# Optimization experiments

Measured on AMD Instinct MI355X. Metric: run time of the kernel, lower is better.

## Reference

```python
import jax, jax.numpy as jnp
import numpy as np

D_MODEL = 256
POOL = 3
SR = 2  # sampling_ratio
TEMP = 10000.0


def pos_grid(D, H, W):
    """2D sine-cos positional encoding, (D,H,W). pos_y channels first, pos_x second."""
    dq = D // 4
    dim_t = TEMP ** (2.0 * (jnp.arange(dq) // 2).astype(jnp.float32) / dq)

    def enc(coord):  # (L,) -> (L, 2*dq), interleaved sin/cos
        p = coord[:, None] / dim_t
        return jnp.stack([jnp.sin(p), jnp.cos(p)], axis=-1).reshape(coord.shape[0], -1)

    py = enc(jnp.linspace(0.0, 1.0, H))  # (H, 2dq)
    px = enc(jnp.linspace(0.0, 1.0, W))  # (W, 2dq)
    pos = jnp.concatenate([
        jnp.broadcast_to(py[:, None, :], (H, W, 2 * dq)),
        jnp.broadcast_to(px[None, :, :], (H, W, 2 * dq)),
    ], axis=-1)  # (H, W, D)
    return jnp.transpose(pos, (2, 0, 1))  # (D, H, W)


def proj_pos(x, Wp, bp):
    """1x1 conv projection to D then add 2D pos enc. x: (B,C,H,W) -> (B,D,H,W)."""
    y = jnp.einsum('bchw,dc->bdhw', x, Wp) + bp[None, :, None, None]
    return y + pos_grid(Wp.shape[0], x.shape[2], x.shape[3])[None]


def roi_align_mean(feat, bidx, boxes, scale):
    """torchvision roi_align (aligned=True, sampling_ratio=SR, output=POOLxPOOL)
    followed by mean over the pooled grid. feat (B,D,H,W), boxes (N,4) xyxy -> (N,D).
    Since every bin averages SR*SR samples, mean over bins == mean over all samples."""
    B, D, H, W = feat.shape
    f = jnp.transpose(feat, (0, 2, 3, 1))  # (B,H,W,D)
    x1 = boxes[:, 0] * scale - 0.5
    y1 = boxes[:, 1] * scale - 0.5
    x2 = boxes[:, 2] * scale - 0.5
    y2 = boxes[:, 3] * scale - 0.5
    bw = (x2 - x1) / POOL
    bh = (y2 - y1) / POOL
    # sample offsets within roi, in units of bin size: (POOL*SR,)
    off = (jnp.arange(POOL, dtype=jnp.float32)[:, None]
           + (jnp.arange(SR, dtype=jnp.float32)[None, :] + 0.5) / SR).reshape(-1)
    ys = y1[:, None] + bh[:, None] * off  # (N,S) with S = POOL*SR
    xs = x1[:, None] + bw[:, None] * off

    def coords(c, size):
        valid = (c >= -1.0) & (c <= size)
        c = jnp.clip(c, 0.0, None)
        cl = jnp.minimum(jnp.floor(c).astype(jnp.int32), size - 1)
        ch = jnp.minimum(cl + 1, size - 1)
        return cl, ch, c - cl, valid

    yl, yh, ly, vy = coords(ys, H)
    xl, xh, lx, vx = coords(xs, W)
    hy, hx = 1.0 - ly, 1.0 - lx

    def gather(yy, xx):  # -> (N,S,S,D)
        return f[bidx[:, None, None], yy[:, :, None], xx[:, None, :]]

    v = (hy[:, :, None, None] * hx[:, None, :, None] * gather(yl, xl)
         + hy[:, :, None, None] * lx[:, None, :, None] * gather(yl, xh)
         + ly[:, :, None, None] * hx[:, None, :, None] * gather(yh, xl)
         + ly[:, :, None, None] * lx[:, None, :, None] * gather(yh, xh))
    mask = (vy[:, :, None] & vx[:, None, :])[..., None]
    v = jnp.where(mask, v, 0.0)
    return v.mean(axis=(1, 2))  # (N, D)


def token_mlp(tok, ln_g, ln_b, W1, b1, W2, b2):
    m = tok.mean(-1, keepdims=True)
    var = jnp.mean((tok - m) ** 2, -1, keepdims=True)
    h = (tok - m) / jnp.sqrt(var + 1e-5) * ln_g + ln_b
    h = jax.nn.gelu(h @ W1.T + b1, approximate=False)  # torch nn.GELU default = exact
    return h @ W2.T + b2


def setup_inputs():
    key = jax.random.key(0)
    ks = jax.random.split(key, 16)
    B, K, D = 8, 100, D_MODEL
    p3 = jax.random.normal(ks[0], (B, 512, 128, 128), jnp.float32)
    p4 = jax.random.normal(ks[1], (B, 1024, 64, 64), jnp.float32)
    p5 = jax.random.normal(ks[2], (B, 2048, 32, 32), jnp.float32)
    # valid xyxy boxes inside a 1024x1024 frame
    x1 = jax.random.uniform(ks[3], (B, K, 1)) * 880.0
    y1 = jax.random.uniform(ks[4], (B, K, 1)) * 880.0
    bw = jax.random.uniform(ks[5], (B, K, 1)) * 128.0 + 8.0
    bh = jax.random.uniform(ks[6], (B, K, 1)) * 128.0 + 8.0
    boxes = jnp.concatenate([x1, y1, x1 + bw, y1 + bh], axis=-1)

    def lin(k, o, i):
        return (jax.random.normal(k, (o, i), jnp.float32) / np.sqrt(i)).astype(jnp.float32)

    return dict(
        p3=p3, p4=p4, p5=p5, boxes=boxes,
        W3=lin(ks[7], D, 512), b3=jnp.zeros((D,), jnp.float32),
        W4=lin(ks[8], D, 1024), b4=jnp.zeros((D,), jnp.float32),
        W5=lin(ks[9], D, 2048), b5=jnp.zeros((D,), jnp.float32),
        ln_g=jnp.ones((D,), jnp.float32), ln_b=jnp.zeros((D,), jnp.float32),
        W1=lin(ks[10], D, D), b1=jnp.zeros((D,), jnp.float32),
        W2=lin(ks[11], D, D), b2=jnp.zeros((D,), jnp.float32),
        input_w=1024, input_h=1024,
    )


def reference(p3, p4, p5, boxes, W3, b3, W4, b4, W5, b5, ln_g, ln_b, W1, b1, W2, b2, input_w, input_h):
    B, K = boxes.shape[0], boxes.shape[1]
    bidx = jnp.repeat(jnp.arange(B, dtype=jnp.int32), K)  # (B*K,)
    flat = boxes.reshape(-1, 4)
    tok = jnp.zeros((B * K, D_MODEL), jnp.float32)
    for feat, Wp, bp in ((p3, W3, b3), (p4, W4, b4), (p5, W5, b5)):
        y = proj_pos(feat, Wp, bp)
        s = min(y.shape[3] / (input_w + 1e-6), y.shape[2] / (input_h + 1e-6))
        tok = tok + roi_align_mean(y, bidx, flat, s)
    tok = token_mlp(tok, ln_g, ln_b, W1, b1, W2, b2)
    return tok.reshape(B, K, D_MODEL)
```

## Files before the change

### kernel.cpp

```cpp
#include <hip/hip_runtime.h>
#include <hip/hip_fp16.h>
#include <math.h>

#ifndef INT_MAX
#define INT_MAX 0x7fffffff
#endif

typedef __attribute__((ext_vector_type(8))) _Float16 f16x8;
typedef __attribute__((ext_vector_type(4))) float   f32x4;


__device__ __forceinline__ float gelu_exact(float x) {
    return 0.5f * x * (1.0f + erff(x * 0.70710678118654752f));
}

__global__ __launch_bounds__(256)
void build_wt3_kernel(const float* __restrict__ W3, const float* __restrict__ W4,
                      const float* __restrict__ W5, const float* __restrict__ W1,
                      const float* __restrict__ W2,
                      __half* __restrict__ WF3, __half* __restrict__ WF4,
                      __half* __restrict__ WF5,
                      float* __restrict__ W1T, float* __restrict__ W2T)
{
    const int bidx = blockIdx.x;
    const int tid  = threadIdx.x;
    if (bidx < 448) {
        const int c = bidx * 256 + tid;
        const float* Wsrc; __half* dst; int K, c0;
        if (c < 16384)      { Wsrc = W3; dst = WF3; K = 512;  c0 = c; }
        else if (c < 49152) { Wsrc = W4; dst = WF4; K = 1024; c0 = c - 16384; }
        else                { Wsrc = W5; dst = WF5; K = 2048; c0 = c - 49152; }
        const int t  = c0 >> 10;
        const int r  = c0 & 1023;
        const int d  = r >> 2;
        const int lg = r & 3;
        const float* src = Wsrc + (size_t)d * K + t * 32 + lg * 8;
        f16x8 hv;
        #pragma unroll
        for (int j = 0; j < 8; ++j) hv[j] = (_Float16)src[j];
        *(f16x8*)(dst + (size_t)c0 * 8) = hv;
    } else if (bidx < 704) {
        const int k = bidx - 448;
        W1T[(size_t)k * 256 + tid] = W1[(size_t)tid * 256 + k];
    } else {
        const int k = bidx - 704;
        W2T[(size_t)k * 256 + tid] = W2[(size_t)tid * 256 + k];
    }
}

__global__ __launch_bounds__(256)
void roi_setup2_kernel(const float* __restrict__ boxes,
                       const float* __restrict__ b3, const float* __restrict__ b4,
                       const float* __restrict__ b5,
                       const int* __restrict__ iw_p, const int* __restrict__ ih_p,
                       float* __restrict__ SREC, float* __restrict__ P)
{
    const int n   = blockIdx.x;
    const int s   = blockIdx.y;
    const int tid = threadIdx.x;

    int H, W;
    const float* bp;
    if (s == 0)      { H = 128; W = 128; bp = b3; }
    else if (s == 1) { H = 64;  W = 64;  bp = b4; }
    else             { H = 32;  W = 32;  bp = b5; }

    __shared__ float wy[32];
    __shared__ float wx[48];
    __shared__ int   sh_r0, sh_rs, sh_x0, sh_xs;
    __shared__ float sh_syc, sh_sxc;

    if (tid < 32)              wy[tid]      = 0.0f;
    if (tid >= 32 && tid < 80) wx[tid - 32] = 0.0f;
    __syncthreads();

    const float scale = fminf((float)W / ((float)(*iw_p) + 1e-6f),
                              (float)H / ((float)(*ih_p) + 1e-6f));
    float* rec = &SREC[(size_t)(n * 3 + s) * 64];

    if (tid == 0) {
        float c1 = boxes[(size_t)n * 4 + 1] * scale - 0.5f;
        float c2 = boxes[(size_t)n * 4 + 3] * scale - 0.5f;
        float bs = (c2 - c1) / 3.0f;
        int   yls[6], yhs[6], vv[6];
        float lys[6];
        int r0 = INT_MAX; float cnt = 0.0f;
        #pragma unroll
        for (int i = 0; i < 6; ++i) {
            float off = 0.25f + 0.5f * (float)i;
            float ys  = c1 + bs * off;
            int v = (ys >= -1.0f) && (ys <= (float)H);
            float yc = fmaxf(ys, 0.0f);
            int yl = (int)floorf(yc); if (yl > H - 1) yl = H - 1;
            int yh = yl + 1;          if (yh > H - 1) yh = H - 1;
            float ly = yc - (float)yl;
            yls[i] = yl; yhs[i] = yh; lys[i] = ly; vv[i] = v;
            if (v) { r0 = min(r0, yl); cnt += 1.0f; }
        }
        if (r0 == INT_MAX) r0 = 0;
        int rmax = 0;
        #pragma unroll
        for (int i = 0; i < 6; ++i) if (vv[i]) {
            int a = min(yls[i] - r0, 31);
            int h = min(yhs[i] - r0, 31);
            wy[a] += 1.0f - lys[i];
            wy[h] += lys[i];
            rmax = max(rmax, h);
        }
        sh_r0 = r0; sh_rs = rmax + 1; sh_syc = cnt;
        int cntn = 0;
        for (int r = 0; r <= rmax && cntn < 12; ++r) {
            if (wy[r] != 0.0f) {
                rec[4 + cntn]  = (float)(r0 + r);
                rec[16 + cntn] = wy[r];
                ++cntn;
            }
        }
        rec[0] = (float)cntn;
    }
    if (tid == 1) {
        float c1 = boxes[(size_t)n * 4 + 0] * scale - 0.5f;
        float c2 = boxes[(size_t)n * 4 + 2] * scale - 0.5f;
        float bs = (c2 - c1) / 3.0f;
        int   xls[6], xhs[6], vv[6];
        float lxs[6];
        int x0r = INT_MAX; float cnt = 0.0f;
        #pragma unroll
        for (int i = 0; i < 6; ++i) {
            float off = 0.25f + 0.5f * (float)i;
            float xs  = c1 + bs * off;
            int v = (xs >= -1.0f) && (xs <= (float)W);
            float xc = fmaxf(xs, 0.0f);
            int xl = (int)floorf(xc); if (xl > W - 1) xl = W - 1;
            int xh = xl + 1;          if (xh > W - 1) xh = W - 1;
            float lx = xc - (float)xl;
            xls[i] = xl; xhs[i] = xh; lxs[i] = lx; vv[i] = v;
            if (v) { x0r = min(x0r, xl); cnt += 1.0f; }
        }
        if (x0r == INT_MAX) x0r = 0;
        int imax = 0;
        #pragma unroll
        for (int i = 0; i < 6; ++i) if (vv[i]) {
            int a = min(xls[i] - x0r, 47);
            int h = min(xhs[i] - x0r, 47);
            wx[a] += 1.0f - lxs[i];
            wx[h] += lxs[i];
            imax = max(imax, h);
        }
        sh_x0 = x0r; sh_xs = imax + 1; sh_sxc = cnt;
        int cntn = 0;
        for (int j = 0; j <= imax && cntn < 12; ++j) {
            if (wx[j] != 0.0f) {
                rec[28 + cntn] = (float)(x0r + j);
                rec[40 + cntn] = wx[j];
                ++cntn;
            }
        }
        rec[1] = (float)cntn;
    }
    __syncthreads();

    const int r0 = sh_r0, rs = sh_rs, x0 = sh_x0, xsr = sh_xs;

    {
        const int d = tid;
        const float syc = sh_syc, sxc = sh_sxc;
        float val;
        if (d < 128) {
            int   t     = d >> 2;
            float invf  = expf(-(float)t * (logf(10000.0f) / 32.0f));
            float istep = 1.0f / (float)(H - 1);
            float sum = 0.0f;
            for (int r = 0; r < rs; ++r) {
                float w = wy[r];
                if (w != 0.0f) {
                    float ang = (float)(r0 + r) * istep * invf;
                    float sn, cs; sincosf(ang, &sn, &cs);
                    sum = fmaf(w, (d & 1) ? cs : sn, sum);
                }
            }
            val = sxc * sum;
        } else {
            int   d2    = d - 128;
            int   t     = d2 >> 2;
            float invf  = expf(-(float)t * (logf(10000.0f) / 32.0f));
            float istep = 1.0f / (float)(W - 1);
            float sum = 0.0f;
            for (int j = 0; j < xsr; ++j) {
                float w = wx[j];
                if (w != 0.0f) {
                    float ang = (float)(x0 + j) * istep * invf;
                    float sn, cs; sincosf(ang, &sn, &cs);
                    sum = fmaf(w, (d & 1) ? cs : sn, sum);
                }
            }
            val = syc * sum;
        }
        float cnt = syc * sxc;
        P[((size_t)n * 3 + s) * 256 + d] = (val + cnt * bp[d]) * (1.0f / 36.0f);
    }
}

__global__ __launch_bounds__(512, 2)
void proj5_kernel(const float* __restrict__ p3, const float* __restrict__ p4,
                  const float* __restrict__ p5,
                  const __half* __restrict__ WF3, const __half* __restrict__ WF4,
                  const __half* __restrict__ WF5,
                  __half* __restrict__ F3, __half* __restrict__ F4,
                  __half* __restrict__ F5,
                  int n5, int n4)
{
    const int bid = blockIdx.x;
    const float* feat; const __half* WF; __half* F;
    int C, HW, m0;
    if (bid < n5)           { C = 2048; HW = 1024;  feat = p5; WF = WF5; F = F5; m0 = bid * 64; }
    else if (bid < n5 + n4) { C = 1024; HW = 4096;  feat = p4; WF = WF4; F = F4; m0 = (bid - n5) * 64; }
    else                    { C = 512;  HW = 16384; feat = p3; WF = WF3; F = F3; m0 = (bid - n5 - n4) * 64; }

    const int tid = threadIdx.x;
    const int wv  = tid >> 6;
    const int l   = tid & 63;
    const int lm  = l & 15;
    const int lg  = l >> 4;
    const int dq  = wv & 3;
    const int ph  = wv >> 2;
    const int b    = m0 / HW;
    const int pos0 = m0 % HW;
    const int nk   = C >> 5;

    const float* a0 = feat + (size_t)b * C * HW + pos0 + ph * 32 + lm;
    const float* a1 = a0 + 16;
    const __half* wbase = WF + ((size_t)(dq * 64 + lm) * 4 + lg) * 8;

    f32x4 acc[8];
    #pragma unroll
    for (int i = 0; i < 8; ++i) acc[i] = (f32x4){0.f, 0.f, 0.f, 0.f};

    float a0c[8], a1c[8], a0n[8], a1n[8];
    f16x8 bc[4], bn[4];

    #pragma unroll
    for (int j = 0; j < 8; ++j) {
        const size_t ko = (size_t)(lg * 8 + j) * HW;
        a0c[j] = a0[ko]; a1c[j] = a1[ko];
    }
    #pragma unroll
    for (int j = 0; j < 8; ++j) {
        const size_t ko = (size_t)(32 + lg * 8 + j) * HW;
        a0n[j] = a0[ko]; a1n[j] = a1[ko];
    }
    #pragma unroll
    for (int nt = 0; nt < 4; ++nt) bc[nt] = *(const f16x8*)(wbase + nt * 512);
    #pragma unroll
    for (int nt = 0; nt < 4; ++nt) bn[nt] = *(const f16x8*)(wbase + 8192 + nt * 512);

    for (int t = 0; t < nk; t += 2) {
        {
            f16x8 af0, af1;
            #pragma unroll
            for (int j = 0; j < 8; ++j) {
                af0[j] = (_Float16)a0c[j];
                af1[j] = (_Float16)a1c[j];
            }
            if (t + 2 < nk) {
                const int k0 = (t + 2) * 32;
                #pragma unroll
                for (int j = 0; j < 8; ++j) {
                    const size_t ko = (size_t)(k0 + lg * 8 + j) * HW;
                    a0c[j] = a0[ko]; a1c[j] = a1[ko];
                }
            }
            #pragma unroll
            for (int nt = 0; nt < 4; ++nt) {
                acc[nt]     = __builtin_amdgcn_mfma_f32_16x16x32_f16(af0, bc[nt], acc[nt],     0, 0, 0);
                acc[nt + 4] = __builtin_amdgcn_mfma_f32_16x16x32_f16(af1, bc[nt], acc[nt + 4], 0, 0, 0);
            }
            if (t + 2 < nk) {
                const __half* wb = wbase + (size_t)(t + 2) * 8192;
                #pragma unroll
                for (int nt = 0; nt < 4; ++nt) bc[nt] = *(const f16x8*)(wb + nt * 512);
            }
        }
        {
            f16x8 af0, af1;
            #pragma unroll
            for (int j = 0; j < 8; ++j) {
                af0[j] = (_Float16)a0n[j];
                af1[j] = (_Float16)a1n[j];
            }
            if (t + 3 < nk) {
                const int k0 = (t + 3) * 32;
                #pragma unroll
                for (int j = 0; j < 8; ++j) {
                    const size_t ko = (size_t)(k0 + lg * 8 + j) * HW;
                    a0n[j] = a0[ko]; a1n[j] = a1[ko];
                }
            }
            #pragma unroll
            for (int nt = 0; nt < 4; ++nt) {
                acc[nt]     = __builtin_amdgcn_mfma_f32_16x16x32_f16(af0, bn[nt], acc[nt],     0, 0, 0);
                acc[nt + 4] = __builtin_amdgcn_mfma_f32_16x16x32_f16(af1, bn[nt], acc[nt + 4], 0, 0, 0);
            }
            if (t + 3 < nk) {
                const __half* wb = wbase + (size_t)(t + 3) * 8192;
                #pragma unroll
                for (int nt = 0; nt < 4; ++nt) bn[nt] = *(const f16x8*)(wb + nt * 512);
            }
        }
    }

    #pragma unroll
    for (int mt = 0; mt < 2; ++mt) {
        #pragma unroll
        for (int nt = 0; nt < 4; ++nt) {
            #pragma unroll
            for (int i = 0; i < 4; ++i) {
                const int px = pos0 + ph * 32 + mt * 16 + lg * 4 + i;
                const int d  = dq * 64 + nt * 16 + lm;
                F[((size_t)b * HW + px) * 256 + d] = __float2half(acc[nt + mt * 4][i]);
            }
        }
    }
}

__global__ __launch_bounds__(256)
void sample2_kernel(const __half* __restrict__ F3, const __half* __restrict__ F4,
                    const __half* __restrict__ F5,
                    const float* __restrict__ SREC, const float* __restrict__ P,
                    float* __restrict__ tokp, int K100)
{
    const int n = blockIdx.x;
    const int s = blockIdx.y;
    const int d = threadIdx.x;
    const int b = n / K100;

    __shared__ float rsh[64];
    if (d < 64) rsh[d] = SREC[(size_t)(n * 3 + s) * 64 + d];
    __syncthreads();

    const __half* F; int HW, W;
    if (s == 0)      { F = F3; HW = 16384; W = 128; }
    else if (s == 1) { F = F4; HW = 4096;  W = 64; }
    else             { F = F5; HW = 1024;  W = 32; }

    const int ny = (int)rsh[0];
    const int nx = (int)rsh[1];
    const size_t base = (size_t)b * HW * 256 + d;

    float acc = 0.0f;
    for (int i = 0; i < ny; ++i) {
        const int   row = (int)rsh[4 + i];
        const float wyv = rsh[16 + i];
        const size_t rb = base + (size_t)(row * W) * 256;
        float rsum = 0.0f;
        for (int j = 0; j < nx; ++j) {
            const int   col = (int)rsh[28 + j];
            const float wxv = rsh[40 + j];
            rsum = fmaf(wxv, __half2float(F[rb + (size_t)col * 256]), rsum);
        }
        acc = fmaf(wyv, rsum, acc);
    }
    tokp[(size_t)(n * 3 + s) * 256 + d] = acc * (1.0f / 36.0f)
                                        + P[(size_t)(n * 3 + s) * 256 + d];
}

__global__ __launch_bounds__(256)
void mlp2_kernel(const float* __restrict__ tokp,
                 const float* __restrict__ lng, const float* __restrict__ lnb,
                 const float* __restrict__ W1T, const float* __restrict__ b1,
                 const float* __restrict__ W2T, const float* __restrict__ b2,
                 float* __restrict__ out, int N)
{
    const int n0  = blockIdx.x * 8;
    const int tid = threadIdx.x;

    __shared__ float tokl[8][257];
    __shared__ float hl[8][257];
    __shared__ float mval[8], rstd[8];

    #pragma unroll
    for (int t = 0; t < 8; ++t) {
        const size_t nb = (size_t)(n0 + t) * 3 * 256 + tid;
        tokl[t][tid] = tokp[nb] + tokp[nb + 256] + tokp[nb + 512];
    }
    __syncthreads();

    const int wv = tid >> 6, lane = tid & 63;
    for (int t = wv; t < 8; t += 4) {
        float x0 = tokl[t][lane], x1 = tokl[t][lane + 64];
        float x2 = tokl[t][lane + 128], x3 = tokl[t][lane + 192];
        float sm = x0 + x1 + x2 + x3;
        float sq = x0 * x0 + x1 * x1 + x2 * x2 + x3 * x3;
        #pragma unroll
        for (int o = 32; o; o >>= 1) { sm += __shfl_xor(sm, o); sq += __shfl_xor(sq, o); }
        if (lane == 0) {
            float m   = sm * (1.0f / 256.0f);
            float var = sq * (1.0f / 256.0f) - m * m;
            mval[t] = m;
            rstd[t] = rsqrtf(var + 1e-5f);
        }
    }
    __syncthreads();

    const float g = lng[tid], be = lnb[tid];
    #pragma unroll
    for (int t = 0; t < 8; ++t)
        hl[t][tid] = (tokl[t][tid] - mval[t]) * rstd[t] * g + be;
    __syncthreads();

    float acc[8];
    const float bb1 = b1[tid];
    #pragma unroll
    for (int t = 0; t < 8; ++t) acc[t] = bb1;
    for (int k = 0; k < 256; ++k) {
        float w = W1T[(size_t)k * 256 + tid];
        #pragma unroll
        for (int t = 0; t < 8; ++t) acc[t] = fmaf(hl[t][k], w, acc[t]);
    }
    __syncthreads();
    #pragma unroll
    for (int t = 0; t < 8; ++t) tokl[t][tid] = gelu_exact(acc[t]);
    __syncthreads();

    const float bb2 = b2[tid];
    #pragma unroll
    for (int t = 0; t < 8; ++t) acc[t] = bb2;
    for (int k = 0; k < 256; ++k) {
        float w = W2T[(size_t)k * 256 + tid];
        #pragma unroll
        for (int t = 0; t < 8; ++t) acc[t] = fmaf(tokl[t][k], w, acc[t]);
    }
    #pragma unroll
    for (int t = 0; t < 8; ++t)
        out[(size_t)(n0 + t) * 256 + tid] = acc[t];
}


__global__ __launch_bounds__(256)
void build_wt_kernel(const float* __restrict__ W3, const float* __restrict__ W4,
                     const float* __restrict__ W5, const float* __restrict__ W1,
                     const float* __restrict__ W2,
                     float* __restrict__ WT, float* __restrict__ W1T,
                     float* __restrict__ W2T)
{
    int k = blockIdx.x;
    int d = threadIdx.x;
    if (k < 512)       WT[(size_t)k * 256 + d]          = W3[(size_t)d * 512  + k];
    else if (k < 1536) WT[(size_t)k * 256 + d]          = W4[(size_t)d * 1024 + (k - 512)];
    else if (k < 3584) WT[(size_t)k * 256 + d]          = W5[(size_t)d * 2048 + (k - 1536)];
    else if (k < 3840) W1T[(size_t)(k - 3584) * 256 + d] = W1[(size_t)d * 256 + (k - 3584)];
    else               W2T[(size_t)(k - 3840) * 256 + d] = W2[(size_t)d * 256 + (k - 3840)];
}

__global__ __launch_bounds__(256)
void roi_setup_kernel(const float* __restrict__ boxes,
                      const float* __restrict__ b3, const float* __restrict__ b4,
                      const float* __restrict__ b5,
                      const int* __restrict__ iw_p, const int* __restrict__ ih_p,
                      float* __restrict__ WREC, float* __restrict__ P)
{
    const int n   = blockIdx.x;
    const int s   = blockIdx.y;
    const int tid = threadIdx.x;

    int H, W;
    const float* bp;
    if (s == 0)      { H = 128; W = 128; bp = b3; }
    else if (s == 1) { H = 64;  W = 64;  bp = b4; }
    else             { H = 32;  W = 32;  bp = b5; }

    __shared__ float wy[32];
    __shared__ float wx[48];
    __shared__ int   sh_r0, sh_rs, sh_x0, sh_nc;
    __shared__ float sh_syc, sh_sxc;

    if (tid < 32)                 wy[tid]      = 0.0f;
    if (tid >= 32 && tid < 80)    wx[tid - 32] = 0.0f;
    __syncthreads();

    const float scale = fminf((float)W / ((float)(*iw_p) + 1e-6f),
                              (float)H / ((float)(*ih_p) + 1e-6f));

    if (tid == 0) {
        float c1 = boxes[(size_t)n * 4 + 1] * scale - 0.5f;
        float c2 = boxes[(size_t)n * 4 + 3] * scale - 0.5f;
        float bs = (c2 - c1) / 3.0f;
        int   yls[6], yhs[6], vv[6];
        float lys[6];
        int r0 = INT_MAX; float cnt = 0.0f;
        #pragma unroll
        for (int i = 0; i < 6; ++i) {
            float off = 0.25f + 0.5f * (float)i;
            float ys  = c1 + bs * off;
            int v = (ys >= -1.0f) && (ys <= (float)H);
            float yc = fmaxf(ys, 0.0f);
            int yl = (int)floorf(yc); if (yl > H - 1) yl = H - 1;
            int yh = yl + 1;          if (yh > H - 1) yh = H - 1;
            float ly = yc - (float)yl;
            yls[i] = yl; yhs[i] = yh; lys[i] = ly; vv[i] = v;
            if (v) { r0 = min(r0, yl); cnt += 1.0f; }
        }
        if (r0 == INT_MAX) r0 = 0;
        int rmax = 0;
        #pragma unroll
        for (int i = 0; i < 6; ++i) if (vv[i]) {
            int a = min(yls[i] - r0, 31);
            int h = min(yhs[i] - r0, 31);
            wy[a] += 1.0f - lys[i];
            wy[h] += lys[i];
            rmax = max(rmax, h);
        }
        sh_r0 = r0; sh_rs = rmax + 1; sh_syc = cnt;
    }
    if (tid == 1) {
        float c1 = boxes[(size_t)n * 4 + 0] * scale - 0.5f;
        float c2 = boxes[(size_t)n * 4 + 2] * scale - 0.5f;
        float bs = (c2 - c1) / 3.0f;
        int   xls[6], xhs[6], vv[6];
        float lxs[6];
        int x0r = INT_MAX; float cnt = 0.0f;
        #pragma unroll
        for (int i = 0; i < 6; ++i) {
            float off = 0.25f + 0.5f * (float)i;
            float xs  = c1 + bs * off;
            int v = (xs >= -1.0f) && (xs <= (float)W);
            float xc = fmaxf(xs, 0.0f);
            int xl = (int)floorf(xc); if (xl > W - 1) xl = W - 1;
            int xh = xl + 1;          if (xh > W - 1) xh = W - 1;
            float lx = xc - (float)xl;
            xls[i] = xl; xhs[i] = xh; lxs[i] = lx; vv[i] = v;
            if (v) { x0r = min(x0r, xl); cnt += 1.0f; }
        }
        if (x0r == INT_MAX) x0r = 0;
        int x0 = x0r & ~15;
        int imax = 0;
        #pragma unroll
        for (int i = 0; i < 6; ++i) if (vv[i]) {
            int a = min(xls[i] - x0, 47);
            int h = min(xhs[i] - x0, 47);
            wx[a] += 1.0f - lxs[i];
            wx[h] += lxs[i];
            imax = max(imax, h);
        }
        int nc = imax / 16 + 1;
        int ncmax = (W - x0) >> 4;
        nc = min(nc, ncmax);
        sh_x0 = x0; sh_nc = max(nc, 1); sh_sxc = cnt;
    }
    __syncthreads();

    const int r0 = sh_r0, rs = sh_rs, x0 = sh_x0, nc = sh_nc;

    float* rec = &WREC[(size_t)(n * 3 + s) * 96];
    if (tid < 32)                 rec[tid]      = wy[tid];
    else if (tid < 80)            rec[tid]      = wx[tid - 32];
    else if (tid == 80)           rec[80]       = (float)r0;
    else if (tid == 81)           rec[81]       = (float)rs;
    else if (tid == 82)           rec[82]       = (float)x0;
    else if (tid == 83)           rec[83]       = (float)nc;
    else if (tid == 84)           rec[84]       = sh_syc;
    else if (tid == 85)           rec[85]       = sh_sxc;

    {
        const int d = tid;
        const float syc = sh_syc, sxc = sh_sxc;
        float val;
        if (d < 128) {
            int   t     = d >> 2;
            float invf  = expf(-(float)t * (logf(10000.0f) / 32.0f));
            float istep = 1.0f / (float)(H - 1);
            float sum = 0.0f;
            for (int r = 0; r < rs; ++r) {
                float w = wy[r];
                float ang = (float)(r0 + r) * istep * invf;
                float sn, cs; sincosf(ang, &sn, &cs);
                sum = fmaf(w, (d & 1) ? cs : sn, sum);
            }
            val = sxc * sum;
        } else {
            int   d2    = d - 128;
            int   t     = d2 >> 2;
            float invf  = expf(-(float)t * (logf(10000.0f) / 32.0f));
            float istep = 1.0f / (float)(W - 1);
            float sum = 0.0f;
            int nx = nc << 4;
            for (int j = 0; j < nx; ++j) {
                float w = wx[j];
                if (w != 0.0f) {
                    float ang = (float)(x0 + j) * istep * invf;
                    float sn, cs; sincosf(ang, &sn, &cs);
                    sum = fmaf(w, (d & 1) ? cs : sn, sum);
                }
            }
            val = syc * sum;
        }
        float cnt = syc * sxc;
        P[((size_t)n * 3 + s) * 256 + d] = (val + cnt * bp[d]) * (1.0f / 36.0f);
    }
}

__global__ __launch_bounds__(256)
void roi_gather_kernel(const float* __restrict__ p3, const float* __restrict__ p4,
                       const float* __restrict__ p5,
                       const float* __restrict__ WREC,
                       float* __restrict__ G, int K)
{
    const int yc  = blockIdx.x;
    const int n   = blockIdx.y;
    const int tid = threadIdx.x;

    int s, chunk;
    if (yc < 8)       { s = 0; chunk = yc; }
    else if (yc < 24) { s = 1; chunk = yc - 8; }
    else              { s = 2; chunk = yc - 24; }

    int C, H, W, koff;
    const float* feat;
    if (s == 0)      { C = 512;  H = 128; W = 128; koff = 0;    feat = p3; }
    else if (s == 1) { C = 1024; H = 64;  W = 64;  koff = 512;  feat = p4; }
    else             { C = 2048; H = 32;  W = 32;  koff = 1536; feat = p5; }
    const int HW = H * W;
    const int b  = n / K;

    __shared__ float sh[96];
    if (tid < 96) sh[tid] = WREC[(size_t)(n * 3 + s) * 96 + tid];
    __syncthreads();

    const int r0 = (int)sh[80];
    const int rs = (int)sh[81];
    const int x0 = (int)sh[82];
    const int nc = (int)sh[83];

    const int c    = chunk * 64 + (tid >> 2);
    const int slot = tid & 3;

    const float* fp = feat + (size_t)b * C * HW + (size_t)c * HW
                    + (size_t)r0 * W + x0 + slot * 4;

    float acc = 0.0f;
    for (int ch = 0; ch < nc; ++ch) {
        const float4 wxv = *(const float4*)&sh[32 + (ch << 4) + slot * 4];
        const float* a = fp + (ch << 4);
        float4 ra = make_float4(0.f, 0.f, 0.f, 0.f);
        int r = 0;
        for (; r + 4 <= rs; r += 4) {
            const float4 v0 = *(const float4*)(a + (size_t)(r + 0) * W);
            const float4 v1 = *(const float4*)(a + (size_t)(r + 1) * W);
            const float4 v2 = *(const float4*)(a + (size_t)(r + 2) * W);
            const float4 v3 = *(const float4*)(a + (size_t)(r + 3) * W);
            const float w0 = sh[r], w1 = sh[r + 1], w2 = sh[r + 2], w3 = sh[r + 3];
            ra.x = fmaf(w0, v0.x, ra.x); ra.y = fmaf(w0, v0.y, ra.y);
            ra.z = fmaf(w0, v0.z, ra.z); ra.w = fmaf(w0, v0.w, ra.w);
            ra.x = fmaf(w1, v1.x, ra.x); ra.y = fmaf(w1, v1.y, ra.y);
            ra.z = fmaf(w1, v1.z, ra.z); ra.w = fmaf(w1, v1.w, ra.w);
            ra.x = fmaf(w2, v2.x, ra.x); ra.y = fmaf(w2, v2.y, ra.y);
            ra.z = fmaf(w2, v2.z, ra.z); ra.w = fmaf(w2, v2.w, ra.w);
            ra.x = fmaf(w3, v3.x, ra.x); ra.y = fmaf(w3, v3.y, ra.y);
            ra.z = fmaf(w3, v3.z, ra.z); ra.w = fmaf(w3, v3.w, ra.w);
        }
        for (; r < rs; ++r) {
            const float4 v = *(const float4*)(a + (size_t)r * W);
            const float w = sh[r];
            ra.x = fmaf(w, v.x, ra.x); ra.y = fmaf(w, v.y, ra.y);
            ra.z = fmaf(w, v.z, ra.z); ra.w = fmaf(w, v.w, ra.w);
        }
        float dsum = ra.x * wxv.x + ra.y * wxv.y + ra.z * wxv.z + ra.w * wxv.w;
        acc += dsum;
    }
    acc += __shfl_xor(acc, 1, 4);
    acc += __shfl_xor(acc, 2, 4);
    if (slot == 0)
        G[(size_t)n * 3584 + koff + c] = acc * (1.0f / 36.0f);
}

__global__ __launch_bounds__(256)
void proj_gemm_kernel(const float* __restrict__ G, const float* __restrict__ WT,
                      float* __restrict__ part, int N)
{
    const int n0  = blockIdx.x * 8;
    const int kc  = blockIdx.y;
    const int tid = threadIdx.x;

    __shared__ float gl[8][128];
    float acc[8];
    #pragma unroll
    for (int t = 0; t < 8; ++t) acc[t] = 0.0f;

    const int kbase = kc * 512;
    const int lt  = tid >> 5;
    const int lc  = (tid & 31) * 4;

    for (int sub = 0; sub < 4; ++sub) {
        const float4 g4 = *(const float4*)&G[(size_t)(n0 + lt) * 3584 + kbase + sub * 128 + lc];
        *(float4*)&gl[lt][lc] = g4;
        __syncthreads();
        const float* wtp = &WT[(size_t)(kbase + sub * 128) * 256 + tid];
        #pragma unroll 4
        for (int k = 0; k < 128; ++k) {
            float w = wtp[(size_t)k * 256];
            #pragma unroll
            for (int t = 0; t < 8; ++t) acc[t] = fmaf(gl[t][k], w, acc[t]);
        }
        __syncthreads();
    }
    #pragma unroll
    for (int t = 0; t < 8; ++t)
        part[((size_t)kc * N + n0 + t) * 256 + tid] = acc[t];
}

__global__ __launch_bounds__(256)
void mlp_kernel(const float* __restrict__ part, const float* __restrict__ P,
                const float* __restrict__ lng, const float* __restrict__ lnb,
                const float* __restrict__ W1T, const float* __restrict__ b1,
                const float* __restrict__ W2T, const float* __restrict__ b2,
                float* __restrict__ out, int N)
{
    const int n0  = blockIdx.x * 8;
    const int tid = threadIdx.x;

    __shared__ float tokl[8][257];
    __shared__ float hl[8][257];
    __shared__ float mval[8], rstd[8];

    #pragma unroll
    for (int t = 0; t < 8; ++t) {
        const int n = n0 + t;
        float v = 0.0f;
        #pragma unroll
        for (int c = 0; c < 7; ++c) v += part[((size_t)c * N + n) * 256 + tid];
        #pragma unroll
        for (int s = 0; s < 3; ++s) v += P[((size_t)n * 3 + s) * 256 + tid];
        tokl[t][tid] = v;
    }
    __syncthreads();

    const int wv = tid >> 6, lane = tid & 63;
    for (int t = wv; t < 8; t += 4) {
        float x0 = tokl[t][lane], x1 = tokl[t][lane + 64];
        float x2 = tokl[t][lane + 128], x3 = tokl[t][lane + 192];
        float sm = x0 + x1 + x2 + x3;
        float sq = x0 * x0 + x1 * x1 + x2 * x2 + x3 * x3;
        #pragma unroll
        for (int o = 32; o; o >>= 1) { sm += __shfl_xor(sm, o); sq += __shfl_xor(sq, o); }
        if (lane == 0) {
            float m   = sm * (1.0f / 256.0f);
            float var = sq * (1.0f / 256.0f) - m * m;
            mval[t] = m;
            rstd[t] = rsqrtf(var + 1e-5f);
        }
    }
    __syncthreads();

    const float g = lng[tid], be = lnb[tid];
    #pragma unroll
    for (int t = 0; t < 8; ++t)
        hl[t][tid] = (tokl[t][tid] - mval[t]) * rstd[t] * g + be;
    __syncthreads();

    float acc[8];
    const float bb1 = b1[tid];
    #pragma unroll
    for (int t = 0; t < 8; ++t) acc[t] = bb1;
    for (int k = 0; k < 256; ++k) {
        float w = W1T[(size_t)k * 256 + tid];
        #pragma unroll
        for (int t = 0; t < 8; ++t) acc[t] = fmaf(hl[t][k], w, acc[t]);
    }
    __syncthreads();
    #pragma unroll
    for (int t = 0; t < 8; ++t) tokl[t][tid] = gelu_exact(acc[t]);
    __syncthreads();

    const float bb2 = b2[tid];
    #pragma unroll
    for (int t = 0; t < 8; ++t) acc[t] = bb2;
    for (int k = 0; k < 256; ++k) {
        float w = W2T[(size_t)k * 256 + tid];
        #pragma unroll
        for (int t = 0; t < 8; ++t) acc[t] = fmaf(tokl[t][k], w, acc[t]);
    }
    #pragma unroll
    for (int t = 0; t < 8; ++t)
        out[(size_t)(n0 + t) * 256 + tid] = acc[t];
}

extern "C" void kernel_launch(void* const* d_in, const int* in_sizes, int n_in,
                              void* d_out, int out_size, void* d_ws, size_t ws_size,
                              hipStream_t stream)
{
    const float* p3    = (const float*)d_in[0];
    const float* p4    = (const float*)d_in[1];
    const float* p5    = (const float*)d_in[2];
    const float* boxes = (const float*)d_in[3];
    const float* W3    = (const float*)d_in[4];
    const float* b3    = (const float*)d_in[5];
    const float* W4    = (const float*)d_in[6];
    const float* b4    = (const float*)d_in[7];
    const float* W5    = (const float*)d_in[8];
    const float* b5    = (const float*)d_in[9];
    const float* lng   = (const float*)d_in[10];
    const float* lnb   = (const float*)d_in[11];
    const float* W1    = (const float*)d_in[12];
    const float* b1    = (const float*)d_in[13];
    const float* W2    = (const float*)d_in[14];
    const float* b2    = (const float*)d_in[15];
    const int*   iw    = (const int*)d_in[16];
    const int*   ih    = (const int*)d_in[17];

    const int B = in_sizes[0] / (512 * 128 * 128);
    const int N = out_size / 256;
    const int K100 = N / B;

    float* out = (float*)d_out;

    const size_t szF3   = (size_t)B * 16384 * 256 * 2;
    const size_t szF4   = (size_t)B * 4096  * 256 * 2;
    const size_t szF5   = (size_t)B * 1024  * 256 * 2;
    const size_t szWF   = (size_t)3584 * 256 * 2;
    const size_t szSREC = (size_t)N * 3 * 64 * 4;
    const size_t szP    = (size_t)N * 3 * 256 * 4;
    const size_t szTok  = (size_t)N * 3 * 256 * 4;
    const size_t szWT12 = (size_t)256 * 256 * 4;
    const size_t need_new = szF3 + szF4 + szF5 + szWF + szSREC + szP + szTok + 2 * szWT12;

    if (ws_size >= need_new) {
        char* w = (char*)d_ws;
        __half* F3   = (__half*)w;            w += szF3;
        __half* F4   = (__half*)w;            w += szF4;
        __half* F5   = (__half*)w;            w += szF5;
        __half* WF   = (__half*)w;            w += szWF;
        float*  SREC = (float*)w;             w += szSREC;
        float*  P    = (float*)w;             w += szP;
        float*  tokp = (float*)w;             w += szTok;
        float*  W1T  = (float*)w;             w += szWT12;
        float*  W2T  = (float*)w;             w += szWT12;

        __half* WF3 = WF;
        __half* WF4 = WF + 131072;
        __half* WF5 = WF + 393216;

        const int n5 = B * 1024  / 64;
        const int n4 = B * 4096  / 64;
        const int n3 = B * 16384 / 64;

        build_wt3_kernel<<<960, 256, 0, stream>>>(W3, W4, W5, W1, W2,
                                                  WF3, WF4, WF5, W1T, W2T);
        roi_setup2_kernel<<<dim3(N, 3), 256, 0, stream>>>(boxes, b3, b4, b5, iw, ih, SREC, P);
        proj5_kernel<<<n5 + n4 + n3, 512, 0, stream>>>(p3, p4, p5, WF3, WF4, WF5,
                                                       F3, F4, F5, n5, n4);
        sample2_kernel<<<dim3(N, 3), 256, 0, stream>>>(F3, F4, F5, SREC, P, tokp, K100);
        mlp2_kernel<<<N / 8, 256, 0, stream>>>(tokp, lng, lnb, W1T, b1, W2T, b2, out, N);
    } else {
        float* G    = (float*)d_ws;
        float* P    = G + (size_t)N * 3584;
        float* WT   = P + (size_t)N * 3 * 256;
        float* W1T  = WT + (size_t)3584 * 256;
        float* W2T  = W1T + (size_t)256 * 256;
        float* part = W2T + (size_t)256 * 256;
        float* WREC = part + (size_t)7 * N * 256;

        build_wt_kernel<<<4096, 256, 0, stream>>>(W3, W4, W5, W1, W2, WT, W1T, W2T);
        roi_setup_kernel<<<dim3(N, 3), 256, 0, stream>>>(boxes, b3, b4, b5, iw, ih, WREC, P);
        roi_gather_kernel<<<dim3(56, N), 256, 0, stream>>>(p3, p4, p5, WREC, G, K100);
        proj_gemm_kernel<<<dim3(N / 8, 7), 256, 0, stream>>>(G, WT, part, N);
        mlp_kernel<<<N / 8, 256, 0, stream>>>(part, P, lng, lnb, W1T, b1, W2T, b2, out, N);
    }
}
```

Baseline: 326.3 us.

## Stage projection activations through LDS via global_load_lds double buffering

The projection GEMM kernel stops loading fp32 activations with strided per-lane global loads into registers. It now uses async global_load_lds copies into a double-buffered shared tile, then reads float4s back out of LDS in MFMA fragment order. The intent is better coalesced global access and fewer registers, which removes the register prefetch arrays. In exchange it adds block-wide barriers on every k-step and drops the min-blocks launch bound, so occupancy and synchronization behavior change.

```diff
diff --git a/kernel.cpp b/kernel.cpp
--- a/kernel.cpp
+++ b/kernel.cpp
@@ -9,6 +9,11 @@
 typedef __attribute__((ext_vector_type(8))) _Float16 f16x8;
 typedef __attribute__((ext_vector_type(4))) float   f32x4;
 
+
+#define GLD4(src, dst)                                                        \
+    __builtin_amdgcn_global_load_lds(                                         \
+        (const __attribute__((address_space(1))) unsigned int*)(const void*)(src), \
+        (__attribute__((address_space(3))) unsigned int*)(void*)(dst), 4, 0, 0)
 
 __device__ __forceinline__ float gelu_exact(float x) {
     return 0.5f * x * (1.0f + erff(x * 0.70710678118654752f));
@@ -201,8 +206,8 @@
     }
 }
 
-__global__ __launch_bounds__(512, 2)
-void proj5_kernel(const float* __restrict__ p3, const float* __restrict__ p4,
+__global__ __launch_bounds__(512)
+void proj6_kernel(const float* __restrict__ p3, const float* __restrict__ p4,
                   const float* __restrict__ p5,
                   const __half* __restrict__ WF3, const __half* __restrict__ WF4,
                   const __half* __restrict__ WF5,
@@ -228,48 +233,63 @@
     const int pos0 = m0 % HW;
     const int nk   = C >> 5;
 
-    const float* a0 = feat + (size_t)b * C * HW + pos0 + ph * 32 + lm;
-    const float* a1 = a0 + 16;
+    __shared__ float sa[2][2048];
+
+    const float* a_st = feat + (size_t)b * C * HW + pos0
+                      + (size_t)(l & 7) * HW + (wv << 3) + (l >> 3);
+    const size_t kstep_str = (size_t)32 * HW;
+    const size_t ktile_str = (size_t)8 * HW;
+
     const __half* wbase = WF + ((size_t)(dq * 64 + lm) * 4 + lg) * 8;
 
+    const int pxq0 = ph * 32 + lm;
+    const int pxq1 = pxq0 + 16;
+    const int ro0 = (((pxq0 >> 3) << 2) + lg) * 64 + ((pxq0 & 7) << 3);
+    const int ro1 = (((pxq1 >> 3) << 2) + lg) * 64 + ((pxq1 & 7) << 3);
+
     f32x4 acc[8];
     #pragma unroll
     for (int i = 0; i < 8; ++i) acc[i] = (f32x4){0.f, 0.f, 0.f, 0.f};
 
-    float a0c[8], a1c[8], a0n[8], a1n[8];
     f16x8 bc[4], bn[4];
 
-    #pragma unroll
-    for (int j = 0; j < 8; ++j) {
-        const size_t ko = (size_t)(lg * 8 + j) * HW;
-        a0c[j] = a0[ko]; a1c[j] = a1[ko];
-    }
-    #pragma unroll
-    for (int j = 0; j < 8; ++j) {
-        const size_t ko = (size_t)(32 + lg * 8 + j) * HW;
-        a0n[j] = a0[ko]; a1n[j] = a1[ko];
+    {
+        const float* s = a_st;
+        float* d0 = &sa[0][(wv * 4) * 64];
+        GLD4(s,                 d0);
+        GLD4(s + ktile_str,     d0 + 64);
+        GLD4(s + 2 * ktile_str, d0 + 128);
+        GLD4(s + 3 * ktile_str, d0 + 192);
     }
     #pragma unroll
     for (int nt = 0; nt < 4; ++nt) bc[nt] = *(const f16x8*)(wbase + nt * 512);
     #pragma unroll
     for (int nt = 0; nt < 4; ++nt) bn[nt] = *(const f16x8*)(wbase + 8192 + nt * 512);
+    __syncthreads();
 
     for (int t = 0; t < nk; t += 2) {
         {
+            const float* s = a_st + (size_t)(t + 1) * kstep_str;
+            float* d0 = &sa[1][(wv * 4) * 64];
+            GLD4(s,                 d0);
+            GLD4(s + ktile_str,     d0 + 64);
+            GLD4(s + 2 * ktile_str, d0 + 128);
+            GLD4(s + 3 * ktile_str, d0 + 192);
+
+            const float* bufc = sa[0];
+            const float4 va = *(const float4*)(bufc + ro0);
+            const float4 vb = *(const float4*)(bufc + ro0 + 4);
+            const float4 vc = *(const float4*)(bufc + ro1);
+            const float4 vd = *(const float4*)(bufc + ro1 + 4);
             f16x8 af0, af1;
-            #pragma unroll
-            for (int j = 0; j < 8; ++j) {
-                af0[j] = (_Float16)a0c[j];
-                af1[j] = (_Float16)a1c[j];
-            }
-            if (t + 2 < nk) {
-                const int k0 = (t + 2) * 32;
-                #pragma unroll
-                for (int j = 0; j < 8; ++j) {
-                    const size_t ko = (size_t)(k0 + lg * 8 + j) * HW;
-                    a0c[j] = a0[ko]; a1c[j] = a1[ko];
-                }
-            }
+            af0[0] = (_Float16)va.x; af0[1] = (_Float16)va.y;
+            af0[2] = (_Float16)va.z; af0[3] = (_Float16)va.w;
+            af0[4] = (_Float16)vb.x; af0[5] = (_Float16)vb.y;
+            af0[6] = (_Float16)vb.z; af0[7] = (_Float16)vb.w;
+            af1[0] = (_Float16)vc.x; af1[1] = (_Float16)vc.y;
+            af1[2] = (_Float16)vc.z; af1[3] = (_Float16)vc.w;
+            af1[4] = (_Float16)vd.x; af1[5] = (_Float16)vd.y;
+            af1[6] = (_Float16)vd.z; af1[7] = (_Float16)vd.w;
             #pragma unroll
             for (int nt = 0; nt < 4; ++nt) {
                 acc[nt]     = __builtin_amdgcn_mfma_f32_16x16x32_f16(af0, bc[nt], acc[nt],     0, 0, 0);
@@ -280,22 +300,31 @@
                 #pragma unroll
                 for (int nt = 0; nt < 4; ++nt) bc[nt] = *(const f16x8*)(wb + nt * 512);
             }
+            __syncthreads();
         }
         {
+            if (t + 2 < nk) {
+                const float* s = a_st + (size_t)(t + 2) * kstep_str;
+                float* d0 = &sa[0][(wv * 4) * 64];
+                GLD4(s,                 d0);
+                GLD4(s + ktile_str,     d0 + 64);
+                GLD4(s + 2 * ktile_str, d0 + 128);
+                GLD4(s + 3 * ktile_str, d0 + 192);
+            }
+            const float* bufc = sa[1];
+            const float4 va = *(const float4*)(bufc + ro0);
+            const float4 vb = *(const float4*)(bufc + ro0 + 4);
+            const float4 vc = *(const float4*)(bufc + ro1);
+            const float4 vd = *(const float4*)(bufc + ro1 + 4);
             f16x8 af0, af1;
-            #pragma unroll
-            for (int j = 0; j < 8; ++j) {
-                af0[j] = (_Float16)a0n[j];
-                af1[j] = (_Float16)a1n[j];
-            }
-            if (t + 3 < nk) {
-                const int k0 = (t + 3) * 32;
-                #pragma unroll
-                for (int j = 0; j < 8; ++j) {
-                    const size_t ko = (size_t)(k0 + lg * 8 + j) * HW;
-                    a0n[j] = a0[ko]; a1n[j] = a1[ko];
-                }
-            }
+            af0[0] = (_Float16)va.x; af0[1] = (_Float16)va.y;
+            af0[2] = (_Float16)va.z; af0[3] = (_Float16)va.w;
+            af0[4] = (_Float16)vb.x; af0[5] = (_Float16)vb.y;
+            af0[6] = (_Float16)vb.z; af0[7] = (_Float16)vb.w;
+            af1[0] = (_Float16)vc.x; af1[1] = (_Float16)vc.y;
+            af1[2] = (_Float16)vc.z; af1[3] = (_Float16)vc.w;
+            af1[4] = (_Float16)vd.x; af1[5] = (_Float16)vd.y;
+            af1[6] = (_Float16)vd.z; af1[7] = (_Float16)vd.w;
             #pragma unroll
             for (int nt = 0; nt < 4; ++nt) {
                 acc[nt]     = __builtin_amdgcn_mfma_f32_16x16x32_f16(af0, bn[nt], acc[nt],     0, 0, 0);
@@ -306,6 +335,7 @@
                 #pragma unroll
                 for (int nt = 0; nt < 4; ++nt) bn[nt] = *(const f16x8*)(wb + nt * 512);
             }
+            __syncthreads();
         }
     }
 
@@ -846,7 +876,7 @@
         build_wt3_kernel<<<960, 256, 0, stream>>>(W3, W4, W5, W1, W2,
                                                   WF3, WF4, WF5, W1T, W2T);
         roi_setup2_kernel<<<dim3(N, 3), 256, 0, stream>>>(boxes, b3, b4, b5, iw, ih, SREC, P);
-        proj5_kernel<<<n5 + n4 + n3, 512, 0, stream>>>(p3, p4, p5, WF3, WF4, WF5,
+        proj6_kernel<<<n5 + n4 + n3, 512, 0, stream>>>(p3, p4, p5, WF3, WF4, WF5,
                                                        F3, F4, F5, n5, n4);
         sample2_kernel<<<dim3(N, 3), 256, 0, stream>>>(F3, F4, F5, SREC, P, tokp, K100);
         mlp2_kernel<<<N / 8, 256, 0, stream>>>(tokp, lng, lnb, W1T, b1, W2T, b2, out, N);
```

After: 341.2 us, median of 2. 1.05x slower.

## Stage projection activations through double-buffered swizzled LDS with float4 global loads

Applied to the files above, without the earlier changes.

In the projection GEMM kernel, each thread used to issue many scalar strided global loads for its MFMA A-fragments. It now loads one float4 of the 32-channel x 64-pixel activation tile per thread, writes it into a double-buffered, XOR-swizzled shared-memory tile, and reads the A-fragments from LDS. The goal is coalesced, vectorised global reads and fewer load instructions. In exchange it adds a barrier per K-step, some LDS traffic and shared-memory use, which could lower occupancy.

```diff
diff --git a/kernel.cpp b/kernel.cpp
--- a/kernel.cpp
+++ b/kernel.cpp
@@ -202,7 +202,7 @@
 }
 
 __global__ __launch_bounds__(512, 2)
-void proj5_kernel(const float* __restrict__ p3, const float* __restrict__ p4,
+void proj8_kernel(const float* __restrict__ p3, const float* __restrict__ p4,
                   const float* __restrict__ p5,
                   const __half* __restrict__ WF3, const __half* __restrict__ WF4,
                   const __half* __restrict__ WF5,
@@ -226,86 +226,86 @@
     const int ph  = wv >> 2;
     const int b    = m0 / HW;
     const int pos0 = m0 % HW;
-    const int nk   = C >> 5;
-
-    const float* a0 = feat + (size_t)b * C * HW + pos0 + ph * 32 + lm;
-    const float* a1 = a0 + 16;
+    const int nsub = C >> 5;
+
+    __shared__ float sa[2][32 * 68];
+
+    const int kk  = tid >> 4;
+    const int pxg = tid & 15;
+    const float* ag = feat + (size_t)b * C * HW + pos0 + pxg * 4 + (size_t)kk * HW;
+    const size_t sstr = (size_t)32 * HW;
+    const int wcol = 4 * (pxg ^ (kk >> 3));
+    const int woff = kk * 68 + wcol;
+
     const __half* wbase = WF + ((size_t)(dq * 64 + lm) * 4 + lg) * 8;
 
+    const int pxq0 = ph * 32 + lm;
+    const int pxq1 = pxq0 + 16;
+    const int rbase0 = lg * 8 * 68 + (pxq0 ^ (4 * lg));
+    const int rbase1 = lg * 8 * 68 + (pxq1 ^ (4 * lg));
+
     f32x4 acc[8];
     #pragma unroll
     for (int i = 0; i < 8; ++i) acc[i] = (f32x4){0.f, 0.f, 0.f, 0.f};
 
-    float a0c[8], a1c[8], a0n[8], a1n[8];
     f16x8 bc[4], bn[4];
-
-    #pragma unroll
-    for (int j = 0; j < 8; ++j) {
-        const size_t ko = (size_t)(lg * 8 + j) * HW;
-        a0c[j] = a0[ko]; a1c[j] = a1[ko];
-    }
-    #pragma unroll
-    for (int j = 0; j < 8; ++j) {
-        const size_t ko = (size_t)(32 + lg * 8 + j) * HW;
-        a0n[j] = a0[ko]; a1n[j] = a1[ko];
-    }
+    float4 vh;
+
+    {
+        const float4 v0 = *(const float4*)ag;
+        *(float4*)&sa[0][woff] = v0;
+    }
+    vh = *(const float4*)(ag + sstr);
     #pragma unroll
     for (int nt = 0; nt < 4; ++nt) bc[nt] = *(const f16x8*)(wbase + nt * 512);
     #pragma unroll
     for (int nt = 0; nt < 4; ++nt) bn[nt] = *(const f16x8*)(wbase + 8192 + nt * 512);
-
-    for (int t = 0; t < nk; t += 2) {
+    __syncthreads();
+
+    for (int s = 0; s < nsub; s += 2) {
         {
+            *(float4*)&sa[1][woff] = vh;
+            if (s + 2 < nsub) vh = *(const float4*)(ag + (size_t)(s + 2) * sstr);
+
+            const float* buf = sa[0];
             f16x8 af0, af1;
             #pragma unroll
-            for (int j = 0; j < 8; ++j) {
-                af0[j] = (_Float16)a0c[j];
-                af1[j] = (_Float16)a1c[j];
-            }
-            if (t + 2 < nk) {
-                const int k0 = (t + 2) * 32;
-                #pragma unroll
-                for (int j = 0; j < 8; ++j) {
-                    const size_t ko = (size_t)(k0 + lg * 8 + j) * HW;
-                    a0c[j] = a0[ko]; a1c[j] = a1[ko];
-                }
-            }
+            for (int j = 0; j < 8; ++j) af0[j] = (_Float16)buf[rbase0 + j * 68];
+            #pragma unroll
+            for (int j = 0; j < 8; ++j) af1[j] = (_Float16)buf[rbase1 + j * 68];
             #pragma unroll
             for (int nt = 0; nt < 4; ++nt) {
                 acc[nt]     = __builtin_amdgcn_mfma_f32_16x16x32_f16(af0, bc[nt], acc[nt],     0, 0, 0);
                 acc[nt + 4] = __builtin_amdgcn_mfma_f32_16x16x32_f16(af1, bc[nt], acc[nt + 4], 0, 0, 0);
             }
-            if (t + 2 < nk) {
-                const __half* wb = wbase + (size_t)(t + 2) * 8192;
+            if (s + 2 < nsub) {
+                const __half* wb = wbase + (size_t)(s + 2) * 8192;
                 #pragma unroll
                 for (int nt = 0; nt < 4; ++nt) bc[nt] = *(const f16x8*)(wb + nt * 512);
             }
+            __syncthreads();
         }
         {
+            if (s + 2 < nsub) *(float4*)&sa[0][woff] = vh;
+            if (s + 3 < nsub) vh = *(const float4*)(ag + (size_t)(s + 3) * sstr);
+
+            const float* buf = sa[1];
             f16x8 af0, af1;
             #pragma unroll
-            for (int j = 0; j < 8; ++j) {
-                af0[j] = (_Float16)a0n[j];
-                af1[j] = (_Float16)a1n[j];
-            }
-            if (t + 3 < nk) {
-                const int k0 = (t + 3) * 32;
-                #pragma unroll
-                for (int j = 0; j < 8; ++j) {
-                    const size_t ko = (size_t)(k0 + lg * 8 + j) * HW;
-                    a0n[j] = a0[ko]; a1n[j] = a1[ko];
-                }
-            }
+            for (int j = 0; j < 8; ++j) af0[j] = (_Float16)buf[rbase0 + j * 68];
+            #pragma unroll
+            for (int j = 0; j < 8; ++j) af1[j] = (_Float16)buf[rbase1 + j * 68];
             #pragma unroll
             for (int nt = 0; nt < 4; ++nt) {
                 acc[nt]     = __builtin_amdgcn_mfma_f32_16x16x32_f16(af0, bn[nt], acc[nt],     0, 0, 0);
                 acc[nt + 4] = __builtin_amdgcn_mfma_f32_16x16x32_f16(af1, bn[nt], acc[nt + 4], 0, 0, 0);
             }
-            if (t + 3 < nk) {
-                const __half* wb = wbase + (size_t)(t + 3) * 8192;
+            if (s + 3 < nsub) {
+                const __half* wb = wbase + (size_t)(s + 3) * 8192;
                 #pragma unroll
                 for (int nt = 0; nt < 4; ++nt) bn[nt] = *(const f16x8*)(wb + nt * 512);
             }
+            __syncthreads();
         }
     }
 
@@ -846,7 +846,7 @@
         build_wt3_kernel<<<960, 256, 0, stream>>>(W3, W4, W5, W1, W2,
                                                   WF3, WF4, WF5, W1T, W2T);
         roi_setup2_kernel<<<dim3(N, 3), 256, 0, stream>>>(boxes, b3, b4, b5, iw, ih, SREC, P);
-        proj5_kernel<<<n5 + n4 + n3, 512, 0, stream>>>(p3, p4, p5, WF3, WF4, WF5,
+        proj8_kernel<<<n5 + n4 + n3, 512, 0, stream>>>(p3, p4, p5, WF3, WF4, WF5,
                                                        F3, F4, F5, n5, n4);
         sample2_kernel<<<dim3(N, 3), 256, 0, stream>>>(F3, F4, F5, SREC, P, tokp, K100);
         mlp2_kernel<<<N / 8, 256, 0, stream>>>(tokp, lng, lnb, W1T, b1, W2T, b2, out, N);
```

New measurement: 285.5 us. -12.5%, faster.
